# Performance work log

Hardware: AMD Instinct MI355X
Metric: run time of the kernel (lower is better)

The kernel has to match this reference:

```python
import jax, jax.numpy as jnp
import numpy as np

N_NODES = 100000


def gcn_conv(x, edge_index, W, b):
    """PyG-style GCNConv: symmetric-normalized A+I propagation of x @ W, plus bias."""
    n = x.shape[0]
    src, dst = edge_index[0], edge_index[1]
    loops = jnp.arange(n, dtype=src.dtype)
    src = jnp.concatenate([src, loops])  # add self loops
    dst = jnp.concatenate([dst, loops])
    deg = jax.ops.segment_sum(jnp.ones_like(src, dtype=x.dtype), dst, num_segments=n)
    dinv = jnp.where(deg > 0, jax.lax.rsqrt(deg), 0.0)
    norm = dinv[src] * dinv[dst]  # [E+n]
    h = x @ W  # [n, out]
    msg = h[src] * norm[:, None]  # gather + scale
    out = jax.ops.segment_sum(msg, dst, num_segments=n)  # scatter-add
    return out + b


def setup_inputs() -> dict:
    key = jax.random.key(0)
    ks = jax.random.split(key, 5)
    x = jax.random.normal(ks[0], (N_NODES, 4), dtype=jnp.float32)
    edge_index = jax.random.randint(ks[1], (2, 3200000), 0, N_NODES, dtype=jnp.int64)
    W1 = jax.random.normal(ks[2], (4, 64), dtype=jnp.float32) * 0.5
    b1 = jnp.zeros((64,), dtype=jnp.float32)
    W2 = jax.random.normal(ks[3], (64, 32), dtype=jnp.float32) * 0.125
    b2 = jnp.zeros((32,), dtype=jnp.float32)
    return {"x": x, "edge_index": edge_index, "W1": W1, "b1": b1, "W2": W2, "b2": b2}


def reference(x, edge_index, W1, b1, W2, b2):
    h = gcn_conv(x, edge_index, W1, b1)
    h = jax.nn.relu(h)
    # F.dropout with training=False is identity (eval-mode reference)
    h = gcn_conv(h, edge_index, W2, b2)
    return jnp.mean(h, axis=0)  # [32]
```

## Files before the change

kernel.cpp:

```cpp
#include <hip/hip_runtime.h>

#define ST 512
#define EPB 8192
#define DT 512
#define MT 1024
#define S_LOG 8
#define S 256
#define CAP 8912
#define MAXB 512

__device__ __forceinline__ void gAtomAdd(float* p, float v) {
    unsafeAtomicAdd(p, v);
}

__global__ void k_init(int* __restrict__ cur_d, int* __restrict__ cur_s,
                       float* __restrict__ g, int nb) {
    int t = threadIdx.x;
    if (t < nb) { cur_d[t] = t * CAP; cur_s[t] = t * CAP; }
    if (t < 64) g[t] = 0.0f;
}

__global__ void __launch_bounds__(ST) k_sctr1(
        const int4* __restrict__ src4, const int4* __restrict__ dst4, int E, int NSB,
        int* __restrict__ cur_d, int* __restrict__ cur_s,
        unsigned* __restrict__ rec_d, unsigned* __restrict__ rec_s, int nb) {
    __shared__ unsigned lrec[EPB];
    __shared__ unsigned short lbkt[EPB];
    __shared__ int cnt[MAXB];
    __shared__ int lst[MAXB];
    __shared__ int gb[MAXB];
    int t = threadIdx.x;
    int ph = blockIdx.x >= NSB;
    int bid = ph ? blockIdx.x - NSB : blockIdx.x;
    const int4* key4 = ph ? src4 : dst4;
    const int4* pay4 = ph ? dst4 : src4;
    int* cursor = ph ? cur_s : cur_d;
    unsigned* rec = ph ? rec_s : rec_d;
    int E4 = E >> 2;
    int b4 = bid * (EPB / 4);
    int m = min(EPB, E - bid * EPB);

    cnt[t] = 0;
    __syncthreads();
    int4 K[4], P[4];
    bool v[4];
    int rk[16];
    #pragma unroll
    for (int k = 0; k < 4; ++k) {
        int idx = b4 + k * ST + t;
        v[k] = idx < E4;
        if (v[k]) { K[k] = key4[idx]; P[k] = pay4[idx]; }
    }
    #pragma unroll
    for (int k = 0; k < 4; ++k) {
        if (v[k]) {
            rk[4 * k + 0] = atomicAdd(&cnt[K[k].x >> S_LOG], 1);
            rk[4 * k + 1] = atomicAdd(&cnt[K[k].y >> S_LOG], 1);
            rk[4 * k + 2] = atomicAdd(&cnt[K[k].z >> S_LOG], 1);
            rk[4 * k + 3] = atomicAdd(&cnt[K[k].w >> S_LOG], 1);
        }
    }
    __syncthreads();
    int c = cnt[t];
    for (int o = 1; o < MAXB; o <<= 1) {
        int u = (t >= o) ? cnt[t - o] : 0;
        __syncthreads();
        cnt[t] += u;
        __syncthreads();
    }
    lst[t] = cnt[t] - c;
    gb[t] = (c > 0) ? atomicAdd(&cursor[t], c) : 0;
    __syncthreads();
    #pragma unroll
    for (int k = 0; k < 4; ++k) {
        if (v[k]) {
            int bb, p;
            bb = K[k].x >> S_LOG; p = lst[bb] + rk[4 * k + 0];
            lrec[p] = ((unsigned)P[k].x << S_LOG) | (unsigned)(K[k].x & (S - 1));
            lbkt[p] = (unsigned short)bb;
            bb = K[k].y >> S_LOG; p = lst[bb] + rk[4 * k + 1];
            lrec[p] = ((unsigned)P[k].y << S_LOG) | (unsigned)(K[k].y & (S - 1));
            lbkt[p] = (unsigned short)bb;
            bb = K[k].z >> S_LOG; p = lst[bb] + rk[4 * k + 2];
            lrec[p] = ((unsigned)P[k].z << S_LOG) | (unsigned)(K[k].z & (S - 1));
            lbkt[p] = (unsigned short)bb;
            bb = K[k].w >> S_LOG; p = lst[bb] + rk[4 * k + 3];
            lrec[p] = ((unsigned)P[k].w << S_LOG) | (unsigned)(K[k].w & (S - 1));
            lbkt[p] = (unsigned short)bb;
        }
    }
    __syncthreads();
    for (int i = t; i < m; i += ST) {
        int bb = lbkt[i];
        rec[gb[bb] + (i - lst[bb])] = lrec[i];
    }
}

__global__ void __launch_bounds__(DT) k_dy(
        const unsigned* __restrict__ rec_d, const int* __restrict__ cur_d,
        const float4* __restrict__ x, float* __restrict__ dinv,
        float4* __restrict__ y, int n) {
    __shared__ int cnt[S];
    int b = blockIdx.x, t = threadIdx.x;
    int lo = b * CAP;
    int md = cur_d[b] - lo;
    if (t < S) cnt[t] = 0;
    __syncthreads();
    int m4 = md >> 2;
    const uint4* r4 = (const uint4*)(rec_d + lo);
    for (int i = t; i < m4; i += DT) {
        uint4 r = r4[i];
        atomicAdd(&cnt[r.x & (S - 1)], 1);
        atomicAdd(&cnt[r.y & (S - 1)], 1);
        atomicAdd(&cnt[r.z & (S - 1)], 1);
        atomicAdd(&cnt[r.w & (S - 1)], 1);
    }
    for (int i = (m4 << 2) + t; i < md; i += DT)
        atomicAdd(&cnt[rec_d[lo + i] & (S - 1)], 1);
    __syncthreads();
    if (t < S) {
        int nd = (b << S_LOG) + t;
        if (nd < n) {
            float dv = rsqrtf((float)cnt[t] + 1.0f);
            dinv[nd] = dv;
            float4 xi = x[nd];
            y[nd] = make_float4(dv * xi.x, dv * xi.y, dv * xi.z, dv * xi.w);
        }
    }
}

__global__ void __launch_bounds__(MT) k_mrg(
        const unsigned* __restrict__ rec_d, const unsigned* __restrict__ rec_s,
        const int* __restrict__ cur_d, const int* __restrict__ cur_s,
        const float4* __restrict__ y, const float* __restrict__ dinv,
        const float* __restrict__ W1, const float* __restrict__ b1,
        float* __restrict__ g, int n) {
    __shared__ unsigned lrec[CAP];
    __shared__ int cnt[S], nst[S];
    __shared__ float sd[S];
    __shared__ float4 lp1[S];
    __shared__ float red[MT];
    int b = blockIdx.x, t = threadIdx.x;
    int lo = b * CAP;
    int md = cur_d[b] - lo;
    if (t < S) { cnt[t] = 0; sd[t] = 0.0f; }
    __syncthreads();
    unsigned rv[9]; int rr[9];
    #pragma unroll
    for (int k = 0; k < 9; ++k) {
        int i = t + k * MT;
        if (i < md) {
            unsigned r = rec_d[lo + i];
            rv[k] = r;
            rr[k] = atomicAdd(&cnt[r & (S - 1)], 1);
        }
    }
    __syncthreads();
    int deg = (t < S) ? cnt[t] : 0;
    for (int o = 1; o < S; o <<= 1) {
        int u = (t < S && t >= o) ? cnt[t - o] : 0;
        __syncthreads();
        if (t < S) cnt[t] += u;
        __syncthreads();
    }
    if (t < S) nst[t] = cnt[t] - deg;
    __syncthreads();
    #pragma unroll
    for (int k = 0; k < 9; ++k) {
        int i = t + k * MT;
        if (i < md) lrec[nst[rv[k] & (S - 1)] + rr[k]] = rv[k] >> S_LOG;
    }
    {
        int ms = cur_s[b] - lo;
        int m4 = ms >> 2;
        const uint4* r4 = (const uint4*)(rec_s + lo);
        for (int i = t; i < m4; i += MT) {
            uint4 r = r4[i];
            float d0 = dinv[r.x >> S_LOG], d1 = dinv[r.y >> S_LOG];
            float d2 = dinv[r.z >> S_LOG], d3 = dinv[r.w >> S_LOG];
            atomicAdd(&sd[r.x & (S - 1)], d0);
            atomicAdd(&sd[r.y & (S - 1)], d1);
            atomicAdd(&sd[r.z & (S - 1)], d2);
            atomicAdd(&sd[r.w & (S - 1)], d3);
        }
        for (int i = (m4 << 2) + t; i < ms; i += MT) {
            unsigned r = rec_s[lo + i];
            atomicAdd(&sd[r & (S - 1)], dinv[r >> S_LOG]);
        }
    }
    __syncthreads();
    int node = t >> 2, q = t & 3;
    int nd = (b << S_LOG) + node;
    if (nd < n) {
        int j = nst[node] + q;
        int j1 = cnt[node];
        float a0 = 0.0f, a1 = 0.0f, a2 = 0.0f, a3 = 0.0f;
        for (; j + 28 < j1; j += 32) {
            int s0 = lrec[j],      s1 = lrec[j + 4],  s2 = lrec[j + 8],  s3 = lrec[j + 12];
            int s4 = lrec[j + 16], s5 = lrec[j + 20], s6 = lrec[j + 24], s7 = lrec[j + 28];
            float4 y0 = y[s0], y1 = y[s1], y2 = y[s2], y3 = y[s3];
            float4 y4 = y[s4], y5 = y[s5], y6 = y[s6], y7 = y[s7];
            a0 += (y0.x + y1.x) + (y2.x + y3.x) + (y4.x + y5.x) + (y6.x + y7.x);
            a1 += (y0.y + y1.y) + (y2.y + y3.y) + (y4.y + y5.y) + (y6.y + y7.y);
            a2 += (y0.z + y1.z) + (y2.z + y3.z) + (y4.z + y5.z) + (y6.z + y7.z);
            a3 += (y0.w + y1.w) + (y2.w + y3.w) + (y4.w + y5.w) + (y6.w + y7.w);
        }
        for (; j + 12 < j1; j += 16) {
            int s0 = lrec[j], s1 = lrec[j + 4], s2 = lrec[j + 8], s3 = lrec[j + 12];
            float4 y0 = y[s0], y1 = y[s1], y2 = y[s2], y3 = y[s3];
            a0 += (y0.x + y1.x) + (y2.x + y3.x);
            a1 += (y0.y + y1.y) + (y2.y + y3.y);
            a2 += (y0.z + y1.z) + (y2.z + y3.z);
            a3 += (y0.w + y1.w) + (y2.w + y3.w);
        }
        for (; j < j1; j += 4) {
            float4 ys = y[lrec[j]];
            a0 += ys.x; a1 += ys.y; a2 += ys.z; a3 += ys.w;
        }
        a0 += __shfl_down(a0, 2); a1 += __shfl_down(a1, 2);
        a2 += __shfl_down(a2, 2); a3 += __shfl_down(a3, 2);
        a0 += __shfl_down(a0, 1); a1 += __shfl_down(a1, 1);
        a2 += __shfl_down(a2, 1); a3 += __shfl_down(a3, 1);
        if (q == 0) {
            float di = dinv[nd];
            lp1[node] = make_float4(di * a0, di * a1, di * a2, di * a3);
        }
    }
    __syncthreads();
    int c = t & 63, w = t >> 6;
    float w0 = W1[c], w1 = W1[64 + c], w2 = W1[128 + c], w3 = W1[192 + c];
    float bb = b1[c];
    int nb0 = b << S_LOG;
    float facc = 0.0f;
    for (int k = w; k < S; k += 16) {
        int ndk = nb0 + k;
        if (ndk >= n) break;
        float di = dinv[ndk];
        float4 p = lp1[k];
        float4 yi = y[ndk];
        float h0 = fmaf(di, yi.x, p.x);
        float h1 = fmaf(di, yi.y, p.y);
        float h2 = fmaf(di, yi.z, p.z);
        float h3 = fmaf(di, yi.w, p.w);
        float h = fmaf(h0, w0, fmaf(h1, w1, fmaf(h2, w2, fmaf(h3, w3, bb))));
        h = fmaxf(h, 0.0f);
        float wi = fmaf(di, sd[k], di * di);
        facc = fmaf(wi, h, facc);
    }
    red[t] = facc;
    __syncthreads();
    if (t < 64) {
        float s = red[t];
        #pragma unroll
        for (int o = 1; o < 16; ++o) s += red[t + 64 * o];
        gAtomAdd(&g[t], s);
    }
}

__global__ void k_final(const float* __restrict__ g, const float* __restrict__ W2,
                        const float* __restrict__ b2, float* __restrict__ out, float inv_n) {
    int j = threadIdx.x;
    if (j < 32) {
        float a = 0.0f;
        #pragma unroll
        for (int c = 0; c < 64; ++c) a = fmaf(g[c], W2[c * 32 + j], a);
        out[j] = fmaf(a, inv_n, b2[j]);
    }
}

extern "C" void kernel_launch(void* const* d_in, const int* in_sizes, int n_in,
                              void* d_out, int out_size, void* d_ws, size_t ws_size,
                              hipStream_t stream) {
    const float* x  = (const float*)d_in[0];
    const int*   ei = (const int*)d_in[1];
    const float* W1 = (const float*)d_in[2];
    const float* b1 = (const float*)d_in[3];
    const float* W2 = (const float*)d_in[4];
    const float* b2 = (const float*)d_in[5];
    float* out = (float*)d_out;

    int n = in_sizes[0] / 4;
    int E = in_sizes[1] / 2;
    const int* src = ei;
    const int* dst = ei + E;
    int NB = (n + S - 1) >> S_LOG;

    char* ws = (char*)d_ws;
    int* cur_d = (int*)ws;
    int* cur_s = cur_d + 512;
    float* g   = (float*)(cur_s + 512);
    size_t ctrl = 1600;
    unsigned* rec_d = (unsigned*)ws + ctrl;
    unsigned* rec_s = rec_d + (size_t)NB * CAP;
    float* yv   = (float*)(rec_s + (size_t)NB * CAP);
    float* dinv = yv + 4 * (size_t)n;

    int NSB = (E + EPB - 1) / EPB;

    k_init<<<1, 512, 0, stream>>>(cur_d, cur_s, g, NB);
    k_sctr1<<<2 * NSB, ST, 0, stream>>>((const int4*)src, (const int4*)dst, E, NSB,
                                        cur_d, cur_s, rec_d, rec_s, NB);
    k_dy<<<NB, DT, 0, stream>>>(rec_d, cur_d, (const float4*)x, dinv,
                                (float4*)yv, n);
    k_mrg<<<NB, MT, 0, stream>>>(rec_d, rec_s, cur_d, cur_s,
                                 (const float4*)yv, dinv, W1, b1, g, n);
    k_final<<<1, 64, 0, stream>>>(g, W2, b2, out, 1.0f / (float)n);
}
```

Before: 155.1 us.

## Halve node bucket size and fold final projection into last merge block

Node buckets shrink from 256 to 128 nodes, which doubles the bucket count to about 782 and reduces per-bucket edge capacity. The scatter kernel grows to 1024 threads and the merge kernel drops to 512 threads to match. The separate final kernel is removed: the last k_mrg block, found with a global done counter after a threadfence, computes the W2 projection. This saves one launch and gives more, smaller merge blocks for occupancy, at the cost of a larger shared-memory bucket histogram and more global cursor atomics in the scatter.

```diff
diff --git a/kernel.cpp b/kernel.cpp
--- a/kernel.cpp
+++ b/kernel.cpp
@@ -1,23 +1,24 @@
 #include <hip/hip_runtime.h>
 
-#define ST 512
+#define ST 1024
 #define EPB 8192
 #define DT 512
-#define MT 1024
-#define S_LOG 8
-#define S 256
-#define CAP 8912
-#define MAXB 512
+#define MT 512
+#define S_LOG 7
+#define S 128
+#define CAP 4800
+#define MAXB 1024
 
 __device__ __forceinline__ void gAtomAdd(float* p, float v) {
     unsafeAtomicAdd(p, v);
 }
 
 __global__ void k_init(int* __restrict__ cur_d, int* __restrict__ cur_s,
-                       float* __restrict__ g, int nb) {
+                       float* __restrict__ g, int* __restrict__ done, int nb) {
     int t = threadIdx.x;
     if (t < nb) { cur_d[t] = t * CAP; cur_s[t] = t * CAP; }
     if (t < 64) g[t] = 0.0f;
+    if (t == 0) *done = 0;
 }
 
 __global__ void __launch_bounds__(ST) k_sctr1(
@@ -42,17 +43,17 @@
 
     cnt[t] = 0;
     __syncthreads();
-    int4 K[4], P[4];
-    bool v[4];
-    int rk[16];
-    #pragma unroll
-    for (int k = 0; k < 4; ++k) {
+    int4 K[2], P[2];
+    bool v[2];
+    int rk[8];
+    #pragma unroll
+    for (int k = 0; k < 2; ++k) {
         int idx = b4 + k * ST + t;
         v[k] = idx < E4;
         if (v[k]) { K[k] = key4[idx]; P[k] = pay4[idx]; }
     }
     #pragma unroll
-    for (int k = 0; k < 4; ++k) {
+    for (int k = 0; k < 2; ++k) {
         if (v[k]) {
             rk[4 * k + 0] = atomicAdd(&cnt[K[k].x >> S_LOG], 1);
             rk[4 * k + 1] = atomicAdd(&cnt[K[k].y >> S_LOG], 1);
@@ -72,7 +73,7 @@
     gb[t] = (c > 0) ? atomicAdd(&cursor[t], c) : 0;
     __syncthreads();
     #pragma unroll
-    for (int k = 0; k < 4; ++k) {
+    for (int k = 0; k < 2; ++k) {
         if (v[k]) {
             int bb, p;
             bb = K[k].x >> S_LOG; p = lst[bb] + rk[4 * k + 0];
@@ -134,20 +135,23 @@
         const int* __restrict__ cur_d, const int* __restrict__ cur_s,
         const float4* __restrict__ y, const float* __restrict__ dinv,
         const float* __restrict__ W1, const float* __restrict__ b1,
-        float* __restrict__ g, int n) {
+        const float* __restrict__ W2, const float* __restrict__ b2,
+        float* __restrict__ g, int* __restrict__ done, float* __restrict__ out,
+        int n, float inv_n, int nblocks) {
     __shared__ unsigned lrec[CAP];
     __shared__ int cnt[S], nst[S];
     __shared__ float sd[S];
     __shared__ float4 lp1[S];
     __shared__ float red[MT];
+    __shared__ int lastFlag;
     int b = blockIdx.x, t = threadIdx.x;
     int lo = b * CAP;
     int md = cur_d[b] - lo;
     if (t < S) { cnt[t] = 0; sd[t] = 0.0f; }
     __syncthreads();
-    unsigned rv[9]; int rr[9];
-    #pragma unroll
-    for (int k = 0; k < 9; ++k) {
+    unsigned rv[10]; int rr[10];
+    #pragma unroll
+    for (int k = 0; k < 10; ++k) {
         int i = t + k * MT;
         if (i < md) {
             unsigned r = rec_d[lo + i];
@@ -166,7 +170,7 @@
     if (t < S) nst[t] = cnt[t] - deg;
     __syncthreads();
     #pragma unroll
-    for (int k = 0; k < 9; ++k) {
+    for (int k = 0; k < 10; ++k) {
         int i = t + k * MT;
         if (i < md) lrec[nst[rv[k] & (S - 1)] + rr[k]] = rv[k] >> S_LOG;
     }
@@ -232,7 +236,7 @@
     float bb = b1[c];
     int nb0 = b << S_LOG;
     float facc = 0.0f;
-    for (int k = w; k < S; k += 16) {
+    for (int k = w; k < S; k += 8) {
         int ndk = nb0 + k;
         if (ndk >= n) break;
         float di = dinv[ndk];
@@ -252,19 +256,22 @@
     if (t < 64) {
         float s = red[t];
         #pragma unroll
-        for (int o = 1; o < 16; ++o) s += red[t + 64 * o];
+        for (int o = 1; o < 8; ++o) s += red[t + 64 * o];
         gAtomAdd(&g[t], s);
     }
-}
-
-__global__ void k_final(const float* __restrict__ g, const float* __restrict__ W2,
-                        const float* __restrict__ b2, float* __restrict__ out, float inv_n) {
-    int j = threadIdx.x;
-    if (j < 32) {
-        float a = 0.0f;
+    __syncthreads();
+    if (t == 0) {
+        __threadfence();
+        int old = atomicAdd(done, 1);
+        lastFlag = (old == nblocks - 1);
+    }
+    __syncthreads();
+    if (lastFlag && t < 32) {
+        __threadfence();
+        float acc = 0.0f;
         #pragma unroll
-        for (int c = 0; c < 64; ++c) a = fmaf(g[c], W2[c * 32 + j], a);
-        out[j] = fmaf(a, inv_n, b2[j]);
+        for (int cc = 0; cc < 64; ++cc) acc = fmaf(g[cc], W2[cc * 32 + t], acc);
+        out[t] = fmaf(acc, inv_n, b2[t]);
     }
 }
 
@@ -287,9 +294,10 @@
 
     char* ws = (char*)d_ws;
     int* cur_d = (int*)ws;
-    int* cur_s = cur_d + 512;
-    float* g   = (float*)(cur_s + 512);
-    size_t ctrl = 1600;
+    int* cur_s = cur_d + 1024;
+    float* g   = (float*)(cur_s + 1024);
+    int* done  = (int*)(g + 64);
+    size_t ctrl = 2116;
     unsigned* rec_d = (unsigned*)ws + ctrl;
     unsigned* rec_s = rec_d + (size_t)NB * CAP;
     float* yv   = (float*)(rec_s + (size_t)NB * CAP);
@@ -297,12 +305,12 @@
 
     int NSB = (E + EPB - 1) / EPB;
 
-    k_init<<<1, 512, 0, stream>>>(cur_d, cur_s, g, NB);
+    k_init<<<1, 1024, 0, stream>>>(cur_d, cur_s, g, done, NB);
     k_sctr1<<<2 * NSB, ST, 0, stream>>>((const int4*)src, (const int4*)dst, E, NSB,
                                         cur_d, cur_s, rec_d, rec_s, NB);
     k_dy<<<NB, DT, 0, stream>>>(rec_d, cur_d, (const float4*)x, dinv,
                                 (float4*)yv, n);
     k_mrg<<<NB, MT, 0, stream>>>(rec_d, rec_s, cur_d, cur_s,
-                                 (const float4*)yv, dinv, W1, b1, g, n);
-    k_final<<<1, 64, 0, stream>>>(g, W2, b2, out, 1.0f / (float)n);
-}
+                                 (const float4*)yv, dinv, W1, b1, W2, b2,
+                                 g, done, out, n, 1.0f / (float)n, NB);
+}
```

Result: slower. 172.5 us (+11.2%).
